# Performance work log

Hardware: AMD Instinct MI355X
Metric: run time of the kernel (lower is better)

## Reference

```python
import jax, jax.numpy as jnp
import numpy as np

HID = 1024   # hidden_size
NH = 16      # num_heads
HD = HID // NH   # 64 head_dim
RD = int(HD * 0.25)  # 16 rotary_dim
B = 2
S = 2048
ROPE_BASE = 10000.0


def setup_inputs() -> dict:
    key = jax.random.key(0)
    ks = jax.random.split(key, 4)
    hidden_states = jax.random.normal(ks[0], (B, S, HID), jnp.float32)
    # torch nn.Linear weights: [out_features, in_features]
    Wqkv = jax.random.normal(ks[1], (3 * HID, HID), jnp.float32) * (HID ** -0.5)
    bqkv = jnp.zeros((3 * HID,), jnp.float32)
    Wd = jax.random.normal(ks[2], (HID, HID), jnp.float32) * (HID ** -0.5)
    bd = jnp.zeros((HID,), jnp.float32)
    return {"hidden_states": hidden_states, "Wqkv": Wqkv, "bqkv": bqkv, "Wd": Wd, "bd": bd}


def _rotary_tables(seq_len):
    inv_freq = 1.0 / (ROPE_BASE ** (jnp.arange(0, RD, 2, dtype=jnp.float32) / RD))
    t = jnp.arange(seq_len, dtype=jnp.float32)
    freqs = jnp.outer(t, inv_freq)                       # [S, RD/2]
    emb = jnp.concatenate([freqs, freqs], axis=-1)       # [S, RD]
    return jnp.cos(emb)[None, None], jnp.sin(emb)[None, None]  # [1,1,S,RD]


def _rotate_half(x):
    x1, x2 = jnp.split(x, 2, axis=-1)
    return jnp.concatenate([-x2, x1], axis=-1)


def reference(hidden_states, Wqkv, bqkv, Wd, bd):
    b, s, _ = hidden_states.shape
    qkv = hidden_states @ Wqkv.T + bqkv                  # [b,s,3*HID]
    qkv = qkv.reshape(b, s, 3, NH, HD).transpose(2, 0, 3, 1, 4)  # [3,b,nh,s,hd]
    q, k, v = qkv[0], qkv[1], qkv[2]

    cos, sin = _rotary_tables(s)
    q_rot, q_pass = q[..., :RD], q[..., RD:]
    k_rot, k_pass = k[..., :RD], k[..., RD:]
    q_rot = q_rot * cos + _rotate_half(q_rot) * sin
    k_rot = k_rot * cos + _rotate_half(k_rot) * sin
    q = jnp.concatenate([q_rot, q_pass], axis=-1)
    k = jnp.concatenate([k_rot, k_pass], axis=-1)

    scale = HD ** -0.5
    logits = jnp.einsum('bhqd,bhkd->bhqk', q, k) * scale  # [b,nh,s,s]
    causal_mask = jnp.triu(jnp.full((s, s), -jnp.inf, dtype=logits.dtype), 1)
    probs = jax.nn.softmax(logits + causal_mask, axis=-1)

    # KA recurrence: A_i = p_ii * V_i + sum_{j<i} p_ij * A_j
    # <=> (I - strict_lower(P)) A = diag(P) * V  -> batched triangular solve
    L = jnp.eye(s, dtype=probs.dtype) - jnp.tril(probs, -1)      # [b,nh,s,s]
    rhs = jnp.diagonal(probs, axis1=-2, axis2=-1)[..., None] * v  # [b,nh,s,hd]
    A = jax.scipy.linalg.solve_triangular(L, rhs, lower=True)     # [b,nh,s,hd]

    attn_output = A.transpose(0, 2, 1, 3).reshape(b, s, HID)
    return attn_output @ Wd.T + bd
```

## Files before the change

kernel.cpp:

```cpp
#include <hip/hip_runtime.h>
#include <math.h>

namespace {

constexpr int B  = 2, S = 2048, NH = 16, HD = 64, HID = 1024;
constexpr int BH = B * NH;
constexpr int NSTEP2 = 8;

constexpr size_t OFF_A    = 4194304;
constexpr size_t OFF_Q    = 12582912;
constexpr size_t OFF_K    = 16777216;
constexpr size_t OFF_V    = 20971520;
constexpr size_t OFF_ZI   = 25231360;
constexpr size_t OFF_PD   = 25296896;
constexpr size_t OFF_UP   = 25362432;
constexpr size_t WS_FLOATS = 29294592;

typedef __attribute__((ext_vector_type(8))) short bf16x8;
typedef __attribute__((ext_vector_type(4))) float f32x4;

__device__ inline unsigned short bf_rne(float x) {
  const unsigned u = __float_as_uint(x);
  return (unsigned short)((u + 0x7FFFu + ((u >> 16) & 1u)) >> 16);
}
__device__ inline float bf2f(short h) {
  return __uint_as_float((unsigned)(unsigned short)h << 16);
}
__device__ inline void split8(const float4 a, const float4 b,
                              bf16x8& hi, bf16x8& lo) {
  float v[8] = {a.x, a.y, a.z, a.w, b.x, b.y, b.z, b.w};
#pragma unroll
  for (int i = 0; i < 8; ++i) {
    const unsigned short h = bf_rne(v[i]);
    hi[i] = (short)h;
    lo[i] = (short)bf_rne(v[i] - bf2f((short)h));
  }
}
__device__ inline f32x4 apply3(const short* __restrict__ mh_,
                               const short* __restrict__ ml_,
                               const float* __restrict__ brow, int lg) {
  f32x4 o = (f32x4)0.f;
#pragma unroll
  for (int ks = 0; ks < 2; ++ks) {
    const bf16x8 mh = *(const bf16x8*)(mh_ + ks * 32 + lg * 8);
    const bf16x8 ml = *(const bf16x8*)(ml_ + ks * 32 + lg * 8);
    const float* bp = brow + ks * 32 + lg * 8;
    bf16x8 bh, bl;
    split8(*(const float4*)bp, *(const float4*)(bp + 4), bh, bl);
    o = __builtin_amdgcn_mfma_f32_16x16x32_bf16(mh, bh, o, 0, 0, 0);
    o = __builtin_amdgcn_mfma_f32_16x16x32_bf16(ml, bh, o, 0, 0, 0);
    o = __builtin_amdgcn_mfma_f32_16x16x32_bf16(mh, bl, o, 0, 0, 0);
  }
  return o;
}

__global__ __launch_bounds__(256) void split_pre(
    const float* __restrict__ hs, short* __restrict__ h1, short* __restrict__ l1,
    const float* __restrict__ wq, short* __restrict__ h2, short* __restrict__ l2) {
  const int n1 = B * S * HID / 4;
  const int n2 = 3 * HID * HID / 4;
  for (int g = blockIdx.x * 256 + threadIdx.x; g < n1 + n2; g += gridDim.x * 256) {
    const bool first = g < n1;
    const int idx = first ? g : g - n1;
    const float4 x = first ? *(const float4*)(hs + (size_t)idx * 4)
                           : *(const float4*)(wq + (size_t)idx * 4);
    short4 h, l;
    h.x = bf_rne(x.x); h.y = bf_rne(x.y); h.z = bf_rne(x.z); h.w = bf_rne(x.w);
    l.x = bf_rne(x.x - bf2f(h.x));
    l.y = bf_rne(x.y - bf2f(h.y));
    l.z = bf_rne(x.z - bf2f(h.z));
    l.w = bf_rne(x.w - bf2f(h.w));
    if (first) {
      *(short4*)(h1 + (size_t)idx * 4) = h;
      *(short4*)(l1 + (size_t)idx * 4) = l;
    } else {
      *(short4*)(h2 + (size_t)idx * 4) = h;
      *(short4*)(l2 + (size_t)idx * 4) = l;
    }
  }
}

__global__ __launch_bounds__(256) void split_post(
    const float* __restrict__ Abuf, short* __restrict__ h1, short* __restrict__ l1,
    const float* __restrict__ wd, short* __restrict__ h2, short* __restrict__ l2) {
  const int n1 = B * S * HID / 4;
  const int n2 = HID * HID / 4;
  for (int g = blockIdx.x * 256 + threadIdx.x; g < n1 + n2; g += gridDim.x * 256) {
    float4 x;
    if (g < n1) {
      const int m = g >> 8, q = g & 255;
      const int k0 = q * 4;
      const int b = m >> 11, s = m & (S - 1);
      const int h = k0 >> 6, d = k0 & 63;
      x = *(const float4*)(Abuf + (((size_t)(b * NH + h) * S + s) << 6) + d);
    } else {
      x = *(const float4*)(wd + (size_t)(g - n1) * 4);
    }
    short4 h, l;
    h.x = bf_rne(x.x); h.y = bf_rne(x.y); h.z = bf_rne(x.z); h.w = bf_rne(x.w);
    l.x = bf_rne(x.x - bf2f(h.x));
    l.y = bf_rne(x.y - bf2f(h.y));
    l.z = bf_rne(x.z - bf2f(h.z));
    l.w = bf_rne(x.w - bf2f(h.w));
    if (g < n1) {
      *(short4*)(h1 + (size_t)g * 4) = h;
      *(short4*)(l1 + (size_t)g * 4) = l;
    } else {
      *(short4*)(h2 + (size_t)(g - n1) * 4) = h;
      *(short4*)(l2 + (size_t)(g - n1) * 4) = l;
    }
  }
}

__global__ __launch_bounds__(256) void gemm_bf3(
    const short* __restrict__ Ahi, const short* __restrict__ Alo,
    const short* __restrict__ Bhi, const short* __restrict__ Blo,
    const float* __restrict__ bias, float* __restrict__ C,
    int M, int N, int K) {
  __shared__ short ash[128][40], als[128][40], bsh[128][40], bls[128][40];
  const int t = threadIdx.x;
  const int m0 = blockIdx.y * 128, n0 = blockIdx.x * 128;
  const int w = t >> 6, l = t & 63;
  const int wm = (w >> 1) * 64, wn = (w & 1) * 64;
  const int lr = l & 15, lk = (l >> 4) * 8;
  f32x4 acc[4][4];
#pragma unroll
  for (int i = 0; i < 4; ++i)
#pragma unroll
    for (int j = 0; j < 4; ++j) acc[i][j] = (f32x4)0.f;

  for (int kb = 0; kb < K; kb += 32) {
    __syncthreads();
#pragma unroll
    for (int i = 0; i < 2; ++i) {
      const int idx = t + i * 256;
      const int row = idx >> 2, c8 = (idx & 3) * 8;
      *(uint4*)&ash[row][c8] = *(const uint4*)(Ahi + (size_t)(m0 + row) * K + kb + c8);
      *(uint4*)&als[row][c8] = *(const uint4*)(Alo + (size_t)(m0 + row) * K + kb + c8);
      *(uint4*)&bsh[row][c8] = *(const uint4*)(Bhi + (size_t)(n0 + row) * K + kb + c8);
      *(uint4*)&bls[row][c8] = *(const uint4*)(Blo + (size_t)(n0 + row) * K + kb + c8);
    }
    __syncthreads();
    bf16x8 ah[4], al[4], bh[4], bl[4];
#pragma unroll
    for (int mi = 0; mi < 4; ++mi) {
      ah[mi] = *(const bf16x8*)&ash[wm + mi * 16 + lr][lk];
      al[mi] = *(const bf16x8*)&als[wm + mi * 16 + lr][lk];
    }
#pragma unroll
    for (int ni = 0; ni < 4; ++ni) {
      bh[ni] = *(const bf16x8*)&bsh[wn + ni * 16 + lr][lk];
      bl[ni] = *(const bf16x8*)&bls[wn + ni * 16 + lr][lk];
    }
#pragma unroll
    for (int mi = 0; mi < 4; ++mi)
#pragma unroll
      for (int ni = 0; ni < 4; ++ni) {
        acc[mi][ni] = __builtin_amdgcn_mfma_f32_16x16x32_bf16(
            ah[mi], bh[ni], acc[mi][ni], 0, 0, 0);
        acc[mi][ni] = __builtin_amdgcn_mfma_f32_16x16x32_bf16(
            al[mi], bh[ni], acc[mi][ni], 0, 0, 0);
        acc[mi][ni] = __builtin_amdgcn_mfma_f32_16x16x32_bf16(
            ah[mi], bl[ni], acc[mi][ni], 0, 0, 0);
      }
  }
  const int rq = (l >> 4) * 4;
#pragma unroll
  for (int ni = 0; ni < 4; ++ni) {
    const int col = n0 + wn + ni * 16 + lr;
    const float bv = bias[col];
#pragma unroll
    for (int mi = 0; mi < 4; ++mi)
#pragma unroll
      for (int r = 0; r < 4; ++r) {
        const int row = m0 + wm + mi * 16 + rq + r;
        C[(size_t)row * N + col] = acc[mi][ni][r] + bv;
      }
  }
}

__global__ __launch_bounds__(256) void k2_rope(
    const float* __restrict__ qkv, short* __restrict__ Qhi,
    short* __restrict__ Qlo, short* __restrict__ Khi,
    short* __restrict__ Klo, float* __restrict__ V) {
  const int g  = blockIdx.x * 256 + threadIdx.x;
  const int s  = g & (S - 1);
  const int bh = g >> 11;
  const int b  = bh >> 4, h = bh & 15;
  const float* base = qkv + ((size_t)b * S + s) * 3072 + h * 64;
  float q[64], k[64], v[64];
#pragma unroll
  for (int f = 0; f < 16; ++f) {
    const float4 x = *(const float4*)(base + f * 4);
    q[f*4+0]=x.x; q[f*4+1]=x.y; q[f*4+2]=x.z; q[f*4+3]=x.w;
    const float4 y = *(const float4*)(base + 1024 + f * 4);
    k[f*4+0]=y.x; k[f*4+1]=y.y; k[f*4+2]=y.z; k[f*4+3]=y.w;
    const float4 z = *(const float4*)(base + 2048 + f * 4);
    v[f*4+0]=z.x; v[f*4+1]=z.y; v[f*4+2]=z.z; v[f*4+3]=z.w;
  }
  const float PW[8] = {1.0f, 3.1622776601683795f, 10.0f, 31.622776601683793f,
                       100.0f, 316.22776601683796f, 1000.0f, 3162.2776601683795f};
  float qr[16], kr[16];
#pragma unroll
  for (int d = 0; d < 16; ++d) {
    const int j = d & 7;
    const float invf = 1.0f / PW[j];
    const float fr = (float)s * invf;
    float sn, c;
    sincosf(fr, &sn, &c);
    const float rq = (d < 8) ? -q[d + 8] : q[d - 8];
    const float rk = (d < 8) ? -k[d + 8] : k[d - 8];
    qr[d] = q[d] * c + rq * sn;
    kr[d] = k[d] * c + rk * sn;
  }
#pragma unroll
  for (int d = 0; d < 16; ++d) { q[d] = qr[d]; k[d] = kr[d]; }
#pragma unroll
  for (int d = 0; d < 64; ++d) q[d] *= 0.125f;
  const size_t o = ((size_t)bh * S + s) << 6;
  float* vd = V + o;
#pragma unroll
  for (int f = 0; f < 16; ++f) {
    short4 qh, ql, kh, kl;
// ... 181 lines not shown
        const size_t kb = kbase + (((size_t)(16 * ni + lr)) << 6) + ks * 32 + lg * 8;
        const bf16x8 bhf = *(const bf16x8*)(Khi + kb);
        const bf16x8 blf = *(const bf16x8*)(Klo + kb);
        p[ni] = __builtin_amdgcn_mfma_f32_16x16x32_bf16(qfh[ks], bhf, p[ni], 0, 0, 0);
        p[ni] = __builtin_amdgcn_mfma_f32_16x16x32_bf16(qfl[ks], bhf, p[ni], 0, 0, 0);
        p[ni] = __builtin_amdgcn_mfma_f32_16x16x32_bf16(qfh[ks], blf, p[ni], 0, 0, 0);
      }
    }
    const size_t pbase = (((size_t)bh * 16 + (ib >> 1)) * 64) * 64;
#pragma unroll
    for (int ni = 0; ni < 4; ++ni) {
      const int c = 16 * ni + lr;
#pragma unroll
      for (int i = 0; i < 4; ++i) {
        const float val = __expf(p[ni][i]) * ziv[i];
        const unsigned short h = bf_rne(val);
        P10h[pbase + (size_t)(rloc0 + i) * 64 + c] = (short)h;
        P10l[pbase + (size_t)(rloc0 + i) * 64 + c] = (short)bf_rne(val - bf2f((short)h));
      }
    }
  }
  {
    const int c = t & 63, g = t >> 6;
#pragma unroll
    for (int i = 0; i < 16; ++i) {
      const int r = 16 * g + i;
      X[r][c] = (r == c) ? 1.f : 0.f;
    }
  }
  __syncthreads();

  const int c = t & 63, g = t >> 6;
  if (w == 0) {
    for (int rr = 1; rr < 16; ++rr) {
      float a = 0.f;
      for (int j = 0; j < rr; ++j) a += Nb[rr][j] * X[j][l];
      X[rr][l] += a;
    }
  }
  __syncthreads();
#pragma unroll
  for (int I = 1; I < 4; ++I) {
    {
      const int rb4 = 16 * I + 4 * g;
      float s0 = 0.f, s1 = 0.f, s2 = 0.f, s3 = 0.f;
      for (int j = 0; j < 16 * I; j += 4) {
        const float4 n0 = *(const float4*)&Nb[rb4 + 0][j];
        const float4 n1 = *(const float4*)&Nb[rb4 + 1][j];
        const float4 n2 = *(const float4*)&Nb[rb4 + 2][j];
        const float4 n3 = *(const float4*)&Nb[rb4 + 3][j];
        const float x0 = X[j + 0][c], x1 = X[j + 1][c];
        const float x2 = X[j + 2][c], x3 = X[j + 3][c];
        s0 += n0.x * x0 + n0.y * x1 + n0.z * x2 + n0.w * x3;
        s1 += n1.x * x0 + n1.y * x1 + n1.z * x2 + n1.w * x3;
        s2 += n2.x * x0 + n2.y * x1 + n2.z * x2 + n2.w * x3;
        s3 += n3.x * x0 + n3.y * x1 + n3.z * x2 + n3.w * x3;
      }
      X[rb4 + 0][c] += s0; X[rb4 + 1][c] += s1;
      X[rb4 + 2][c] += s2; X[rb4 + 3][c] += s3;
    }
    __syncthreads();
    if (w == 0) {
      const int rb = 16 * I;
      for (int rr = 1; rr < 16; ++rr) {
        const int r = rb + rr;
        float a = 0.f;
        for (int j = rb; j < r; ++j) a += Nb[r][j] * X[j][l];
        X[r][l] += a;
      }
    }
    __syncthreads();
  }

  const size_t mb = (((size_t)bh * 32 + ib) * 64) * 64;
  for (int v = t; v < 4096; v += 256) {
    const int r = v >> 6, cc = v & 63;
    const float x = X[r][cc];
    const unsigned short h = bf_rne(x);
    Mrh[mb + v] = (short)h;
    Mrl[mb + v] = (short)bf_rne(x - bf2f((short)h));
  }
}

__global__ __launch_bounds__(256) void k5_acc(
    const short* __restrict__ Qhi, const short* __restrict__ Qlo,
    const short* __restrict__ Khi, const short* __restrict__ Klo,
    const float* __restrict__ Abuf, const float* __restrict__ zinv,
    float* __restrict__ up, int s) {
  const int bh = blockIdx.z, rh = blockIdx.y, g = blockIdx.x;
  __shared__ float Es[128][68];
  __shared__ float Ats[64][68];
  const int t = threadIdx.x;
  const int w = t >> 6, l = t & 63;
  const int lr = l & 15, lg = l >> 4;
  const int rw = 32 * w;
  const int base = s * 256 + rh * 128;

  bf16x8 qfh[2][2], qfl[2][2];
#pragma unroll
  for (int mi = 0; mi < 2; ++mi)
#pragma unroll
    for (int ks = 0; ks < 2; ++ks) {
      const size_t qo = (((size_t)bh * S + base + rw + mi * 16 + lr) << 6) + ks * 32 + lg * 8;
      qfh[mi][ks] = *(const bf16x8*)(Qhi + qo);
      qfl[mi][ks] = *(const bf16x8*)(Qlo + qo);
    }
  float ziv[2][4];
#pragma unroll
  for (int mi = 0; mi < 2; ++mi)
#pragma unroll
    for (int r = 0; r < 4; ++r)
      ziv[mi][r] = zinv[(size_t)bh * S + base + rw + mi * 16 + lg * 4 + r];

  f32x4 out[2][4];
#pragma unroll
  for (int mi = 0; mi < 2; ++mi)
#pragma unroll
    for (int ni = 0; ni < 4; ++ni) out[mi][ni] = (f32x4)0.f;

  for (int j = g; j < 2 * s; j += 7) {
    for (int h = 0; h < 2; ++h) {
      __syncthreads();
      for (int v = t; v < 1024; v += 256) {
        const int d = v & 63, sq = v >> 6;
        const size_t ab = ((size_t)bh * S + j * 128 + h * 64 + sq * 4) << 6;
        float4 o;
        o.x = Abuf[ab + d];
        o.y = Abuf[ab + 64 + d];
        o.z = Abuf[ab + 128 + d];
        o.w = Abuf[ab + 192 + d];
        *(float4*)&Ats[d][sq * 4] = o;
      }
      f32x4 qk[2][4];
#pragma unroll
      for (int mi = 0; mi < 2; ++mi)
#pragma unroll
        for (int ni = 0; ni < 4; ++ni) qk[mi][ni] = (f32x4)0.f;
#pragma unroll
      for (int ks = 0; ks < 2; ++ks) {
#pragma unroll
        for (int ni = 0; ni < 4; ++ni) {
          const size_t ko = (((size_t)bh * S + j * 128 + h * 64 + ni * 16 + lr) << 6) + ks * 32 + lg * 8;
          const bf16x8 kh8 = *(const bf16x8*)(Khi + ko);
          const bf16x8 kl8 = *(const bf16x8*)(Klo + ko);
#pragma unroll
          for (int mi = 0; mi < 2; ++mi) {
            qk[mi][ni] = __builtin_amdgcn_mfma_f32_16x16x32_bf16(
                qfh[mi][ks], kh8, qk[mi][ni], 0, 0, 0);
            qk[mi][ni] = __builtin_amdgcn_mfma_f32_16x16x32_bf16(
                qfl[mi][ks], kh8, qk[mi][ni], 0, 0, 0);
            qk[mi][ni] = __builtin_amdgcn_mfma_f32_16x16x32_bf16(
                qfh[mi][ks], kl8, qk[mi][ni], 0, 0, 0);
          }
        }
      }
#pragma unroll
      for (int mi = 0; mi < 2; ++mi)
#pragma unroll
        for (int ni = 0; ni < 4; ++ni)
#pragma unroll
          for (int r = 0; r < 4; ++r)
            Es[rw + mi * 16 + lg * 4 + r][ni * 16 + lr] =
                __expf(qk[mi][ni][r]) * ziv[mi][r];
      __syncthreads();
#pragma unroll
      for (int ks = 0; ks < 2; ++ks) {
        bf16x8 eh[2], el[2];
#pragma unroll
        for (int mi = 0; mi < 2; ++mi) {
          const float* ep = &Es[rw + mi * 16 + lr][ks * 32 + lg * 8];
          split8(*(const float4*)ep, *(const float4*)(ep + 4), eh[mi], el[mi]);
        }
#pragma unroll
        for (int ni = 0; ni < 4; ++ni) {
          const float* ap = &Ats[ni * 16 + lr][ks * 32 + lg * 8];
          bf16x8 ah8, al8;
          split8(*(const float4*)ap, *(const float4*)(ap + 4), ah8, al8);
#pragma unroll
          for (int mi = 0; mi < 2; ++mi) {
            out[mi][ni] = __builtin_amdgcn_mfma_f32_16x16x32_bf16(
                eh[mi], ah8, out[mi][ni], 0, 0, 0);
            out[mi][ni] = __builtin_amdgcn_mfma_f32_16x16x32_bf16(
                el[mi], ah8, out[mi][ni], 0, 0, 0);
            out[mi][ni] = __builtin_amdgcn_mfma_f32_16x16x32_bf16(
                eh[mi], al8, out[mi][ni], 0, 0, 0);
          }
        }
      }
    }
  }
  float* ub = up + (((size_t)(bh * 7 + g) * 2 + rh) << 13);
#pragma unroll
  for (int mi = 0; mi < 2; ++mi)
#pragma unroll
    for (int ni = 0; ni < 4; ++ni)
#pragma unroll
      for (int r = 0; r < 4; ++r)
        ub[(size_t)(rw + mi * 16 + lg * 4 + r) * 64 + ni * 16 + lr] =
            out[mi][ni][r];
}

__global__ __launch_bounds__(256) void k5_fin(
    const short* __restrict__ Qhi, const short* __restrict__ Qlo,
    const short* __restrict__ Khi, const short* __restrict__ Klo,
    const float* __restrict__ V, const float* __restrict__ pd,
    const float* __restrict__ zinv, const float* __restrict__ up,
    const short* __restrict__ Mrh, const short* __restrict__ Mrl,
    const short* __restrict__ P10h, const short* __restrict__ P10l,
    float* __restrict__ Abuf, int s) {
  const int d0 = blockIdx.x * 16;
  const int bh = blockIdx.y;
  const int t = threadIdx.x;
  const int w = t >> 6, l = t & 63;
  const int lr = l & 15, lg = l >> 4;
  const int base = s * 256;
  __shared__ float uT[16][260];
  __shared__ float aT[16][132];
  __shared__ float Es[128][68];
  const int ng = (2 * s < 7) ? 2 * s : 7;

  for (int v = t; v < 1024; v += 256) {
    const int r = v >> 2, f = v & 3;
    const int R = base + r;
    const float4 x = *(const float4*)(V + (((size_t)bh * S + R) << 6) + d0 + f * 4);
    const float p = pd[(size_t)bh * S + R];
    float a0 = p * x.x, a1 = p * x.y, a2 = p * x.z, a3 = p * x.w;
    const int rh = r >> 7, rr = r & 127;
    for (int g = 0; g < ng; ++g) {
      const float4 y = *(const float4*)(
          up + (((size_t)(bh * 7 + g) * 2 + rh) << 13) + (rr << 6) + d0 + f * 4);
      a0 += y.x; a1 += y.y; a2 += y.z; a3 += y.w;
    }
    uT[f * 4 + 0][r] = a0; uT[f * 4 + 1][r] = a1;
    uT[f * 4 + 2][r] = a2; uT[f * 4 + 3][r] = a3;
  }
  __syncthreads();
  const size_t mstep = (size_t)bh * 32 + s * 4;
  {
    const size_t mb = ((mstep + 0) * 64 + 16 * w + lr) * 64;
    const f32x4 o = apply3(Mrh + mb, Mrl + mb, &uT[lr][0], lg);
#pragma unroll
    for (int i = 0; i < 4; ++i) {
      const int r = 16 * w + lg * 4 + i;
      Abuf[(((size_t)bh * S + base + r) << 6) + d0 + lr] = o[i];
      aT[lr][r] = o[i];
    }
  }
  __syncthreads();
  {
    const size_t pb = (((size_t)bh * 16 + 2 * s) * 64 + 16 * w + lr) * 64;
    const f32x4 o = apply3(P10h + pb, P10l + pb, &aT[lr][0], lg);
#pragma unroll
    for (int i = 0; i < 4; ++i)
      uT[lr][64 + 16 * w + lg * 4 + i] += o[i];
  }
  __syncthreads();
  {
    const size_t mb = ((mstep + 1) * 64 + 16 * w + lr) * 64;
    const f32x4 o = apply3(Mrh + mb, Mrl + mb, &uT[lr][64], lg);
#pragma unroll
    for (int i = 0; i < 4; ++i) {
      const int r = 16 * w + lg * 4 + i;
      Abuf[(((size_t)bh * S + base + 64 + r) << 6) + d0 + lr] = o[i];
      aT[lr][64 + r] = o[i];
    }
  }
  {
    const int rw = 32 * w;
    bf16x8 qh_[2][2], ql_[2][2];
#pragma unroll
    for (int mi = 0; mi < 2; ++mi)
#pragma unroll
      for (int ks = 0; ks < 2; ++ks) {
        const size_t qo = (((size_t)bh * S + base + 128 + rw + mi * 16 + lr) << 6) + ks * 32 + lg * 8;
        qh_[mi][ks] = *(const bf16x8*)(Qhi + qo);
        ql_[mi][ks] = *(const bf16x8*)(Qlo + qo);
      }
    float zv[2][4];
#pragma unroll
    for (int mi = 0; mi < 2; ++mi)
#pragma unroll
      for (int i = 0; i < 4; ++i)
        zv[mi][i] = zinv[(size_t)bh * S + base + 128 + rw + mi * 16 + lg * 4 + i];
    for (int ch = 0; ch < 2; ++ch) {
      __syncthreads();
      f32x4 qk[2][4];
#pragma unroll
      for (int mi = 0; mi < 2; ++mi)
#pragma unroll
        for (int ni = 0; ni < 4; ++ni) qk[mi][ni] = (f32x4)0.f;
#pragma unroll
      for (int ks = 0; ks < 2; ++ks) {
#pragma unroll
        for (int ni = 0; ni < 4; ++ni) {
          const size_t ko = (((size_t)bh * S + base + ch * 64 + ni * 16 + lr) << 6) + ks * 32 + lg * 8;
          const bf16x8 kh8 = *(const bf16x8*)(Khi + ko);
          const bf16x8 kl8 = *(const bf16x8*)(Klo + ko);
#pragma unroll
          for (int mi = 0; mi < 2; ++mi) {
            qk[mi][ni] = __builtin_amdgcn_mfma_f32_16x16x32_bf16(
                qh_[mi][ks], kh8, qk[mi][ni], 0, 0, 0);
            qk[mi][ni] = __builtin_amdgcn_mfma_f32_16x16x32_bf16(
                ql_[mi][ks], kh8, qk[mi][ni], 0, 0, 0);
            qk[mi][ni] = __builtin_amdgcn_mfma_f32_16x16x32_bf16(
                qh_[mi][ks], kl8, qk[mi][ni], 0, 0, 0);
          }
        }
      }
#pragma unroll
      for (int mi = 0; mi < 2; ++mi)
#pragma unroll
        for (int ni = 0; ni < 4; ++ni)
#pragma unroll
          for (int i = 0; i < 4; ++i)
            Es[rw + mi * 16 + lg * 4 + i][ni * 16 + lr] =
                __expf(qk[mi][ni][i]) * zv[mi][i];
      __syncthreads();
#pragma unroll
      for (int mi = 0; mi < 2; ++mi) {
        f32x4 o = (f32x4)0.f;
#pragma unroll
        for (int kq = 0; kq < 2; ++kq) {
          const float* ep = &Es[rw + mi * 16 + lr][kq * 32 + lg * 8];
          bf16x8 eh, el;
          split8(*(const float4*)ep, *(const float4*)(ep + 4), eh, el);
          const float* ap = &aT[lr][ch * 64 + kq * 32 + lg * 8];
          bf16x8 ah, al;
          split8(*(const float4*)ap, *(const float4*)(ap + 4), ah, al);
          o = __builtin_amdgcn_mfma_f32_16x16x32_bf16(eh, ah, o, 0, 0, 0);
          o = __builtin_amdgcn_mfma_f32_16x16x32_bf16(el, ah, o, 0, 0, 0);
          o = __builtin_amdgcn_mfma_f32_16x16x32_bf16(eh, al, o, 0, 0, 0);
        }
#pragma unroll
        for (int i = 0; i < 4; ++i)
          uT[lr][128 + rw + mi * 16 + lg * 4 + i] += o[i];
      }
    }
  }
  __syncthreads();
  {
    const size_t mb = ((mstep + 2) * 64 + 16 * w + lr) * 64;
    const f32x4 o = apply3(Mrh + mb, Mrl + mb, &uT[lr][128], lg);
#pragma unroll
    for (int i = 0; i < 4; ++i) {
      const int r = 16 * w + lg * 4 + i;
      Abuf[(((size_t)bh * S + base + 128 + r) << 6) + d0 + lr] = o[i];
      aT[lr][r] = o[i];
    }
  }
  __syncthreads();
  {
    const size_t pb = (((size_t)bh * 16 + 2 * s + 1) * 64 + 16 * w + lr) * 64;
    const f32x4 o = apply3(P10h + pb, P10l + pb, &aT[lr][0], lg);
#pragma unroll
    for (int i = 0; i < 4; ++i)
      uT[lr][192 + 16 * w + lg * 4 + i] += o[i];
  }
  __syncthreads();
  {
    const size_t mb = ((mstep + 3) * 64 + 16 * w + lr) * 64;
    const f32x4 o = apply3(Mrh + mb, Mrl + mb, &uT[lr][192], lg);
#pragma unroll
    for (int i = 0; i < 4; ++i) {
      const int r = 16 * w + lg * 4 + i;
      Abuf[(((size_t)bh * S + base + 192 + r) << 6) + d0 + lr] = o[i];
    }
  }
}

}

extern "C" void kernel_launch(void* const* d_in, const int* in_sizes, int n_in,
                              void* d_out, int out_size, void* d_ws, size_t ws_size,
                              hipStream_t stream) {
  const float* hs   = (const float*)d_in[0];
  const float* Wqkv = (const float*)d_in[1];
  const float* bqkv = (const float*)d_in[2];
  const float* Wd   = (const float*)d_in[3];
  const float* bd   = (const float*)d_in[4];
  float* out = (float*)d_out;
  float* W   = (float*)d_ws;
  if (ws_size < WS_FLOATS * sizeof(float)) return;

  float* qkv   = W;
  float* partZ = W;
  float* Abuf  = W + OFF_A;
  short* Qhi   = (short*)(W + OFF_Q);
  short* Qlo   = Qhi + 4194304;
  short* Khi   = (short*)(W + OFF_K);
  short* Klo   = Khi + 4194304;
  float* Vb    = W + OFF_V;
  float* zi    = W + OFF_ZI;
  float* pdg   = W + OFF_PD;
  float* up    = W + OFF_UP;

  char* wsb = (char*)d_ws;
  short* Ahi  = (short*)(wsb + 50331648);
  short* Alo  = Ahi + 4194304;
  short* Whi  = (short*)(wsb + 67108864);
  short* Wlo  = Whi + 3145728;
  short* A2hi = (short*)(wsb + 50331648);
  short* A2lo = A2hi + 4194304;
  short* Wdhi = (short*)(wsb + 67108864);
  short* Wdlo = Wdhi + 1048576;
  short* P10h = (short*)(wsb);
  short* P10l = P10h + 2097152;
  short* Mrh  = (short*)(wsb + 33554432);
  short* Mrl  = Mrh + 4194304;

  split_pre<<<dim3(2048), 256, 0, stream>>>(hs, Ahi, Alo, Wqkv, Whi, Wlo);
  gemm_bf3<<<dim3(24, 32), 256, 0, stream>>>(Ahi, Alo, Whi, Wlo, bqkv, qkv,
                                             B*S, 3*HID, HID);
  k2_rope<<<dim3(BH * S / 256), 256, 0, stream>>>(qkv, Qhi, Qlo, Khi, Klo, Vb);
  k3_scores<<<dim3(16, 16, BH), 256, 0, stream>>>(Qhi, Qlo, Khi, Klo, partZ, pdg);
  k3_reduce<<<dim3(BH * S / 256), 256, 0, stream>>>(partZ, zi, pdg);
  k4_minv<<<dim3(S / 64, BH), 256, 0, stream>>>(Qhi, Qlo, Khi, Klo, zi,
                                                Mrh, Mrl, P10h, P10l);
  for (int s = 0; s < NSTEP2; ++s) {
    if (s > 0) {
      const int ng = (2 * s < 7) ? 2 * s : 7;
      k5_acc<<<dim3(ng, 2, BH), 256, 0, stream>>>(Qhi, Qlo, Khi, Klo, Abuf, zi,
                                                  up, s);
    }
    k5_fin<<<dim3(4, BH), 256, 0, stream>>>(Qhi, Qlo, Khi, Klo, Vb, pdg, zi, up,
                                            Mrh, Mrl, P10h, P10l, Abuf, s);
  }
  split_post<<<dim3(2048), 256, 0, stream>>>(Abuf, A2hi, A2lo, Wd, Wdhi, Wdlo);
  gemm_bf3<<<dim3(8, 32), 256, 0, stream>>>(A2hi, A2lo, Wdhi, Wdlo, bd, out,
                                            B*S, HID, HID);
}
```

Baseline: 692.5 us.

## Fuse bf16 splitting into GEMM loads and merge acc/fin steps via atomic tickets

The separate split_pre/split_post kernels are removed. The GEMM now loads fp32 operands, splits them into hi/lo bf16 while staging to shared memory, and gathers the attention output layout directly for the output projection. The per-step k5_acc and k5_fin launches are merged into one k5_step kernel. In it, the last four blocks to arrive on a per-head atomic counter wait for all partials and then run the finalize stage, so each step needs one launch instead of two. This cuts kernel launches and intermediate global traffic. In exchange it adds split arithmetic inside the GEMM inner loop and a spin-wait that assumes every block of a step is co-resident.

```diff
diff --git a/kernel.cpp b/kernel.cpp
--- a/kernel.cpp
+++ b/kernel.cpp
@@ -54,67 +54,9 @@
   return o;
 }
 
-__global__ __launch_bounds__(256) void split_pre(
-    const float* __restrict__ hs, short* __restrict__ h1, short* __restrict__ l1,
-    const float* __restrict__ wq, short* __restrict__ h2, short* __restrict__ l2) {
-  const int n1 = B * S * HID / 4;
-  const int n2 = 3 * HID * HID / 4;
-  for (int g = blockIdx.x * 256 + threadIdx.x; g < n1 + n2; g += gridDim.x * 256) {
-    const bool first = g < n1;
-    const int idx = first ? g : g - n1;
-    const float4 x = first ? *(const float4*)(hs + (size_t)idx * 4)
-                           : *(const float4*)(wq + (size_t)idx * 4);
-    short4 h, l;
-    h.x = bf_rne(x.x); h.y = bf_rne(x.y); h.z = bf_rne(x.z); h.w = bf_rne(x.w);
-    l.x = bf_rne(x.x - bf2f(h.x));
-    l.y = bf_rne(x.y - bf2f(h.y));
-    l.z = bf_rne(x.z - bf2f(h.z));
-    l.w = bf_rne(x.w - bf2f(h.w));
-    if (first) {
-      *(short4*)(h1 + (size_t)idx * 4) = h;
-      *(short4*)(l1 + (size_t)idx * 4) = l;
-    } else {
-      *(short4*)(h2 + (size_t)idx * 4) = h;
-      *(short4*)(l2 + (size_t)idx * 4) = l;
-    }
-  }
-}
-
-__global__ __launch_bounds__(256) void split_post(
-    const float* __restrict__ Abuf, short* __restrict__ h1, short* __restrict__ l1,
-    const float* __restrict__ wd, short* __restrict__ h2, short* __restrict__ l2) {
-  const int n1 = B * S * HID / 4;
-  const int n2 = HID * HID / 4;
-  for (int g = blockIdx.x * 256 + threadIdx.x; g < n1 + n2; g += gridDim.x * 256) {
-    float4 x;
-    if (g < n1) {
-      const int m = g >> 8, q = g & 255;
-      const int k0 = q * 4;
-      const int b = m >> 11, s = m & (S - 1);
-      const int h = k0 >> 6, d = k0 & 63;
-      x = *(const float4*)(Abuf + (((size_t)(b * NH + h) * S + s) << 6) + d);
-    } else {
-      x = *(const float4*)(wd + (size_t)(g - n1) * 4);
-    }
-    short4 h, l;
-    h.x = bf_rne(x.x); h.y = bf_rne(x.y); h.z = bf_rne(x.z); h.w = bf_rne(x.w);
-    l.x = bf_rne(x.x - bf2f(h.x));
-    l.y = bf_rne(x.y - bf2f(h.y));
-    l.z = bf_rne(x.z - bf2f(h.z));
-    l.w = bf_rne(x.w - bf2f(h.w));
-    if (g < n1) {
-      *(short4*)(h1 + (size_t)g * 4) = h;
-      *(short4*)(l1 + (size_t)g * 4) = l;
-    } else {
-      *(short4*)(h2 + (size_t)(g - n1) * 4) = h;
-      *(short4*)(l2 + (size_t)(g - n1) * 4) = l;
-    }
-  }
-}
-
-__global__ __launch_bounds__(256) void gemm_bf3(
-    const short* __restrict__ Ahi, const short* __restrict__ Alo,
-    const short* __restrict__ Bhi, const short* __restrict__ Blo,
+template<int GATHER>
+__global__ __launch_bounds__(256) void gemm_f32(
+    const float* __restrict__ A, const float* __restrict__ Bm,
     const float* __restrict__ bias, float* __restrict__ C,
     int M, int N, int K) {
   __shared__ short ash[128][40], als[128][40], bsh[128][40], bls[128][40];
@@ -135,10 +77,24 @@
     for (int i = 0; i < 2; ++i) {
       const int idx = t + i * 256;
       const int row = idx >> 2, c8 = (idx & 3) * 8;
-      *(uint4*)&ash[row][c8] = *(const uint4*)(Ahi + (size_t)(m0 + row) * K + kb + c8);
-      *(uint4*)&als[row][c8] = *(const uint4*)(Alo + (size_t)(m0 + row) * K + kb + c8);
-      *(uint4*)&bsh[row][c8] = *(const uint4*)(Bhi + (size_t)(n0 + row) * K + kb + c8);
-      *(uint4*)&bls[row][c8] = *(const uint4*)(Blo + (size_t)(n0 + row) * K + kb + c8);
+      const float* srcA;
+      if (GATHER) {
+        const int m = m0 + row;
+        const int b = m >> 11, ss = m & (S - 1);
+        const int kk = kb + c8;
+        const int h = kk >> 6, d = kk & 63;
+        srcA = A + (((size_t)(b * NH + h) * S + ss) << 6) + d;
+      } else {
+        srcA = A + (size_t)(m0 + row) * K + kb + c8;
+      }
+      bf16x8 hi, lo;
+      split8(*(const float4*)srcA, *(const float4*)(srcA + 4), hi, lo);
+      *(bf16x8*)&ash[row][c8] = hi;
+      *(bf16x8*)&als[row][c8] = lo;
+      const float* srcB = Bm + (size_t)(n0 + row) * K + kb + c8;
+      split8(*(const float4*)srcB, *(const float4*)(srcB + 4), hi, lo);
+      *(bf16x8*)&bsh[row][c8] = hi;
+      *(bf16x8*)&bls[row][c8] = lo;
     }
     __syncthreads();
     bf16x8 ah[4], al[4], bh[4], bl[4];
@@ -486,173 +442,44 @@
   }
 }
 
-__global__ __launch_bounds__(256) void k5_acc(
-    const short* __restrict__ Qhi, const short* __restrict__ Qlo,
-    const short* __restrict__ Khi, const short* __restrict__ Klo,
-    const float* __restrict__ Abuf, const float* __restrict__ zinv,
-    float* __restrict__ up, int s) {
-  const int bh = blockIdx.z, rh = blockIdx.y, g = blockIdx.x;
-  __shared__ float Es[128][68];
-  __shared__ float Ats[64][68];
-  const int t = threadIdx.x;
-  const int w = t >> 6, l = t & 63;
-  const int lr = l & 15, lg = l >> 4;
-  const int rw = 32 * w;
-  const int base = s * 256 + rh * 128;
-
-  bf16x8 qfh[2][2], qfl[2][2];
-#pragma unroll
-  for (int mi = 0; mi < 2; ++mi)
-#pragma unroll
-    for (int ks = 0; ks < 2; ++ks) {
-      const size_t qo = (((size_t)bh * S + base + rw + mi * 16 + lr) << 6) + ks * 32 + lg * 8;
-      qfh[mi][ks] = *(const bf16x8*)(Qhi + qo);
-      qfl[mi][ks] = *(const bf16x8*)(Qlo + qo);
-    }
-  float ziv[2][4];
-#pragma unroll
-  for (int mi = 0; mi < 2; ++mi)
-#pragma unroll
-    for (int r = 0; r < 4; ++r)
-      ziv[mi][r] = zinv[(size_t)bh * S + base + rw + mi * 16 + lg * 4 + r];
-
-  f32x4 out[2][4];
-#pragma unroll
-  for (int mi = 0; mi < 2; ++mi)
-#pragma unroll
-    for (int ni = 0; ni < 4; ++ni) out[mi][ni] = (f32x4)0.f;
-
-  for (int j = g; j < 2 * s; j += 7) {
-    for (int h = 0; h < 2; ++h) {
-      __syncthreads();
-      for (int v = t; v < 1024; v += 256) {
-        const int d = v & 63, sq = v >> 6;
-        const size_t ab = ((size_t)bh * S + j * 128 + h * 64 + sq * 4) << 6;
-        float4 o;
-        o.x = Abuf[ab + d];
-        o.y = Abuf[ab + 64 + d];
-        o.z = Abuf[ab + 128 + d];
-        o.w = Abuf[ab + 192 + d];
-        *(float4*)&Ats[d][sq * 4] = o;
-      }
-      f32x4 qk[2][4];
-#pragma unroll
-      for (int mi = 0; mi < 2; ++mi)
-#pragma unroll
-        for (int ni = 0; ni < 4; ++ni) qk[mi][ni] = (f32x4)0.f;
-#pragma unroll
-      for (int ks = 0; ks < 2; ++ks) {
-#pragma unroll
-        for (int ni = 0; ni < 4; ++ni) {
-          const size_t ko = (((size_t)bh * S + j * 128 + h * 64 + ni * 16 + lr) << 6) + ks * 32 + lg * 8;
-          const bf16x8 kh8 = *(const bf16x8*)(Khi + ko);
-          const bf16x8 kl8 = *(const bf16x8*)(Klo + ko);
-#pragma unroll
-          for (int mi = 0; mi < 2; ++mi) {
-            qk[mi][ni] = __builtin_amdgcn_mfma_f32_16x16x32_bf16(
-                qfh[mi][ks], kh8, qk[mi][ni], 0, 0, 0);
-            qk[mi][ni] = __builtin_amdgcn_mfma_f32_16x16x32_bf16(
-                qfl[mi][ks], kh8, qk[mi][ni], 0, 0, 0);
-            qk[mi][ni] = __builtin_amdgcn_mfma_f32_16x16x32_bf16(
-                qfh[mi][ks], kl8, qk[mi][ni], 0, 0, 0);
-          }
-        }
-      }
-#pragma unroll
-      for (int mi = 0; mi < 2; ++mi)
-#pragma unroll
-        for (int ni = 0; ni < 4; ++ni)
-#pragma unroll
-          for (int r = 0; r < 4; ++r)
-            Es[rw + mi * 16 + lg * 4 + r][ni * 16 + lr] =
-                __expf(qk[mi][ni][r]) * ziv[mi][r];
-      __syncthreads();
-#pragma unroll
-      for (int ks = 0; ks < 2; ++ks) {
-        bf16x8 eh[2], el[2];
-#pragma unroll
-        for (int mi = 0; mi < 2; ++mi) {
-          const float* ep = &Es[rw + mi * 16 + lr][ks * 32 + lg * 8];
-          split8(*(const float4*)ep, *(const float4*)(ep + 4), eh[mi], el[mi]);
-        }
-#pragma unroll
-        for (int ni = 0; ni < 4; ++ni) {
-          const float* ap = &Ats[ni * 16 + lr][ks * 32 + lg * 8];
-          bf16x8 ah8, al8;
-          split8(*(const float4*)ap, *(const float4*)(ap + 4), ah8, al8);
-#pragma unroll
-          for (int mi = 0; mi < 2; ++mi) {
-            out[mi][ni] = __builtin_amdgcn_mfma_f32_16x16x32_bf16(
-                eh[mi], ah8, out[mi][ni], 0, 0, 0);
-            out[mi][ni] = __builtin_amdgcn_mfma_f32_16x16x32_bf16(
-                el[mi], ah8, out[mi][ni], 0, 0, 0);
-            out[mi][ni] = __builtin_amdgcn_mfma_f32_16x16x32_bf16(
-                eh[mi], al8, out[mi][ni], 0, 0, 0);
-          }
-        }
-      }
-    }
-  }
-  float* ub = up + (((size_t)(bh * 7 + g) * 2 + rh) << 13);
-#pragma unroll
-  for (int mi = 0; mi < 2; ++mi)
-#pragma unroll
-    for (int ni = 0; ni < 4; ++ni)
-#pragma unroll
-      for (int r = 0; r < 4; ++r)
-        ub[(size_t)(rw + mi * 16 + lg * 4 + r) * 64 + ni * 16 + lr] =
-            out[mi][ni][r];
-}
-
 __global__ __launch_bounds__(256) void k5_fin(
     const short* __restrict__ Qhi, const short* __restrict__ Qlo,
     const short* __restrict__ Khi, const short* __restrict__ Klo,
     const float* __restrict__ V, const float* __restrict__ pd,
-    const float* __restrict__ zinv, const float* __restrict__ up,
-    const short* __restrict__ Mrh, const short* __restrict__ Mrl,
-    const short* __restrict__ P10h, const short* __restrict__ P10l,
-    float* __restrict__ Abuf, int s) {
+    const float* __restrict__ zinv, const short* __restrict__ Mrh,
+    const short* __restrict__ Mrl, const short* __restrict__ P10h,
+    const short* __restrict__ P10l, float* __restrict__ Abuf) {
   const int d0 = blockIdx.x * 16;
   const int bh = blockIdx.y;
   const int t = threadIdx.x;
   const int w = t >> 6, l = t & 63;
   const int lr = l & 15, lg = l >> 4;
-  const int base = s * 256;
   __shared__ float uT[16][260];
   __shared__ float aT[16][132];
   __shared__ float Es[128][68];
-  const int ng = (2 * s < 7) ? 2 * s : 7;
 
   for (int v = t; v < 1024; v += 256) {
     const int r = v >> 2, f = v & 3;
-    const int R = base + r;
-    const float4 x = *(const float4*)(V + (((size_t)bh * S + R) << 6) + d0 + f * 4);
-    const float p = pd[(size_t)bh * S + R];
-    float a0 = p * x.x, a1 = p * x.y, a2 = p * x.z, a3 = p * x.w;
-    const int rh = r >> 7, rr = r & 127;
-    for (int g = 0; g < ng; ++g) {
-      const float4 y = *(const float4*)(
-          up + (((size_t)(bh * 7 + g) * 2 + rh) << 13) + (rr << 6) + d0 + f * 4);
-      a0 += y.x; a1 += y.y; a2 += y.z; a3 += y.w;
-    }
-    uT[f * 4 + 0][r] = a0; uT[f * 4 + 1][r] = a1;
-    uT[f * 4 + 2][r] = a2; uT[f * 4 + 3][r] = a3;
-  }
-  __syncthreads();
-  const size_t mstep = (size_t)bh * 32 + s * 4;
+    const float4 x = *(const float4*)(V + (((size_t)bh * S + r) << 6) + d0 + f * 4);
+    const float p = pd[(size_t)bh * S + r];
+    uT[f * 4 + 0][r] = p * x.x; uT[f * 4 + 1][r] = p * x.y;
+    uT[f * 4 + 2][r] = p * x.z; uT[f * 4 + 3][r] = p * x.w;
+  }
+  __syncthreads();
+  const size_t mstep = (size_t)bh * 32;
   {
     const size_t mb = ((mstep + 0) * 64 + 16 * w + lr) * 64;
     const f32x4 o = apply3(Mrh + mb, Mrl + mb, &uT[lr][0], lg);
 #pragma unroll
     for (int i = 0; i < 4; ++i) {
       const int r = 16 * w + lg * 4 + i;
-      Abuf[(((size_t)bh * S + base + r) << 6) + d0 + lr] = o[i];
+      Abuf[(((size_t)bh * S + r) << 6) + d0 + lr] = o[i];
       aT[lr][r] = o[i];
     }
   }
   __syncthreads();
   {
-    const size_t pb = (((size_t)bh * 16 + 2 * s) * 64 + 16 * w + lr) * 64;
+    const size_t pb = (((size_t)bh * 16) * 64 + 16 * w + lr) * 64;
     const f32x4 o = apply3(P10h + pb, P10l + pb, &aT[lr][0], lg);
 #pragma unroll
     for (int i = 0; i < 4; ++i)
@@ -665,7 +492,7 @@
 #pragma unroll
     for (int i = 0; i < 4; ++i) {
       const int r = 16 * w + lg * 4 + i;
-      Abuf[(((size_t)bh * S + base + 64 + r) << 6) + d0 + lr] = o[i];
+      Abuf[(((size_t)bh * S + 64 + r) << 6) + d0 + lr] = o[i];
       aT[lr][64 + r] = o[i];
     }
   }
@@ -676,7 +503,7 @@
     for (int mi = 0; mi < 2; ++mi)
 #pragma unroll
       for (int ks = 0; ks < 2; ++ks) {
-        const size_t qo = (((size_t)bh * S + base + 128 + rw + mi * 16 + lr) << 6) + ks * 32 + lg * 8;
+        const size_t qo = (((size_t)bh * S + 128 + rw + mi * 16 + lr) << 6) + ks * 32 + lg * 8;
         qh_[mi][ks] = *(const bf16x8*)(Qhi + qo);
         ql_[mi][ks] = *(const bf16x8*)(Qlo + qo);
       }
@@ -685,7 +512,7 @@
     for (int mi = 0; mi < 2; ++mi)
 #pragma unroll
       for (int i = 0; i < 4; ++i)
-        zv[mi][i] = zinv[(size_t)bh * S + base + 128 + rw + mi * 16 + lg * 4 + i];
+        zv[mi][i] = zinv[(size_t)bh * S + 128 + rw + mi * 16 + lg * 4 + i];
     for (int ch = 0; ch < 2; ++ch) {
       __syncthreads();
       f32x4 qk[2][4];
@@ -697,7 +524,7 @@
       for (int ks = 0; ks < 2; ++ks) {
 #pragma unroll
         for (int ni = 0; ni < 4; ++ni) {
-          const size_t ko = (((size_t)bh * S + base + ch * 64 + ni * 16 + lr) << 6) + ks * 32 + lg * 8;
+          const size_t ko = (((size_t)bh * S + ch * 64 + ni * 16 + lr) << 6) + ks * 32 + lg * 8;
           const bf16x8 kh8 = *(const bf16x8*)(Khi + ko);
           const bf16x8 kl8 = *(const bf16x8*)(Klo + ko);
 #pragma unroll
@@ -748,13 +575,13 @@
 #pragma unroll
     for (int i = 0; i < 4; ++i) {
       const int r = 16 * w + lg * 4 + i;
-      Abuf[(((size_t)bh * S + base + 128 + r) << 6) + d0 + lr] = o[i];
+      Abuf[(((size_t)bh * S + 128 + r) << 6) + d0 + lr] = o[i];
       aT[lr][r] = o[i];
     }
   }
   __syncthreads();
   {
-    const size_t pb = (((size_t)bh * 16 + 2 * s + 1) * 64 + 16 * w + lr) * 64;
+    const size_t pb = (((size_t)bh * 16 + 1) * 64 + 16 * w + lr) * 64;
     const f32x4 o = apply3(P10h + pb, P10l + pb, &aT[lr][0], lg);
 #pragma unroll
     for (int i = 0; i < 4; ++i)
@@ -767,9 +594,303 @@
 #pragma unroll
     for (int i = 0; i < 4; ++i) {
       const int r = 16 * w + lg * 4 + i;
-      Abuf[(((size_t)bh * S + base + 192 + r) << 6) + d0 + lr] = o[i];
-    }
-  }
+      Abuf[(((size_t)bh * S + 192 + r) << 6) + d0 + lr] = o[i];
+    }
+  }
+}
+
+__global__ __launch_bounds__(256) void k5_step(
+    const short* __restrict__ Qhi, const short* __restrict__ Qlo,
+    const short* __restrict__ Khi, const short* __restrict__ Klo,
+    const float* __restrict__ V, const float* __restrict__ pd,
+    const float* __restrict__ zinv, float* __restrict__ up,
+    const short* __restrict__ Mrh, const short* __restrict__ Mrl,
+    const short* __restrict__ P10h, const short* __restrict__ P10l,
+    float* __restrict__ Abuf, int* __restrict__ cnt, int s) {
+  __shared__ float sb[14976];
+  __shared__ int tks;
+#define ES(r, c)  sb[(r) * 68 + (c)]
+#define ATS(d, c) sb[8704 + (d) * 68 + (c)]
+#define UT(dd, r) sb[(dd) * 260 + (r)]
+#define AT(dd, r) sb[4160 + (dd) * 132 + (r)]
+#define EF(r, c)  sb[6272 + (r) * 68 + (c)]
+  const int bh = blockIdx.z, rh = blockIdx.y, g = blockIdx.x;
+  const int ng = gridDim.x;
+  const int t = threadIdx.x;
+  const int w = t >> 6, l = t & 63;
+  const int lr = l & 15, lg = l >> 4;
+  const int rw = 32 * w;
+  const int base = s * 256 + rh * 128;
+
+  bf16x8 qfh[2][2], qfl[2][2];
+#pragma unroll
+  for (int mi = 0; mi < 2; ++mi)
+#pragma unroll
+    for (int ks = 0; ks < 2; ++ks) {
+      const size_t qo = (((size_t)bh * S + base + rw + mi * 16 + lr) << 6) + ks * 32 + lg * 8;
+      qfh[mi][ks] = *(const bf16x8*)(Qhi + qo);
+      qfl[mi][ks] = *(const bf16x8*)(Qlo + qo);
+    }
+  float ziv[2][4];
+#pragma unroll
+  for (int mi = 0; mi < 2; ++mi)
+#pragma unroll
+    for (int r = 0; r < 4; ++r)
+      ziv[mi][r] = zinv[(size_t)bh * S + base + rw + mi * 16 + lg * 4 + r];
+
+  f32x4 out[2][4];
+#pragma unroll
+  for (int mi = 0; mi < 2; ++mi)
+#pragma unroll
+    for (int ni = 0; ni < 4; ++ni) out[mi][ni] = (f32x4)0.f;
+
+  for (int j = g; j < 2 * s; j += 7) {
+    for (int h = 0; h < 2; ++h) {
+      __syncthreads();
+      for (int v = t; v < 1024; v += 256) {
+        const int d = v & 63, sq = v >> 6;
+        const size_t ab = ((size_t)bh * S + j * 128 + h * 64 + sq * 4) << 6;
+        ATS(d, sq * 4 + 0) = Abuf[ab + d];
+        ATS(d, sq * 4 + 1) = Abuf[ab + 64 + d];
+        ATS(d, sq * 4 + 2) = Abuf[ab + 128 + d];
+        ATS(d, sq * 4 + 3) = Abuf[ab + 192 + d];
+      }
+      f32x4 qk[2][4];
+#pragma unroll
+      for (int mi = 0; mi < 2; ++mi)
+#pragma unroll
+        for (int ni = 0; ni < 4; ++ni) qk[mi][ni] = (f32x4)0.f;
+#pragma unroll
+      for (int ks = 0; ks < 2; ++ks) {
+#pragma unroll
+        for (int ni = 0; ni < 4; ++ni) {
+          const size_t ko = (((size_t)bh * S + j * 128 + h * 64 + ni * 16 + lr) << 6) + ks * 32 + lg * 8;
+          const bf16x8 kh8 = *(const bf16x8*)(Khi + ko);
+          const bf16x8 kl8 = *(const bf16x8*)(Klo + ko);
+#pragma unroll
+          for (int mi = 0; mi < 2; ++mi) {
+            qk[mi][ni] = __builtin_amdgcn_mfma_f32_16x16x32_bf16(
+                qfh[mi][ks], kh8, qk[mi][ni], 0, 0, 0);
+            qk[mi][ni] = __builtin_amdgcn_mfma_f32_16x16x32_bf16(
+                qfl[mi][ks], kh8, qk[mi][ni], 0, 0, 0);
+            qk[mi][ni] = __builtin_amdgcn_mfma_f32_16x16x32_bf16(
+                qfh[mi][ks], kl8, qk[mi][ni], 0, 0, 0);
+          }
+        }
+      }
+#pragma unroll
+      for (int mi = 0; mi < 2; ++mi)
+#pragma unroll
+        for (int ni = 0; ni < 4; ++ni)
+#pragma unroll
+          for (int r = 0; r < 4; ++r)
+            ES(rw + mi * 16 + lg * 4 + r, ni * 16 + lr) =
+                __expf(qk[mi][ni][r]) * ziv[mi][r];
+      __syncthreads();
+#pragma unroll
+      for (int ks = 0; ks < 2; ++ks) {
+        bf16x8 eh[2], el[2];
+#pragma unroll
+        for (int mi = 0; mi < 2; ++mi) {
+          const float* ep = &ES(rw + mi * 16 + lr, ks * 32 + lg * 8);
+          split8(*(const float4*)ep, *(const float4*)(ep + 4), eh[mi], el[mi]);
+        }
+#pragma unroll
+        for (int ni = 0; ni < 4; ++ni) {
+          const float* ap = &ATS(ni * 16 + lr, ks * 32 + lg * 8);
+          bf16x8 ah8, al8;
+          split8(*(const float4*)ap, *(const float4*)(ap + 4), ah8, al8);
+#pragma unroll
+          for (int mi = 0; mi < 2; ++mi) {
+            out[mi][ni] = __builtin_amdgcn_mfma_f32_16x16x32_bf16(
+                eh[mi], ah8, out[mi][ni], 0, 0, 0);
+            out[mi][ni] = __builtin_amdgcn_mfma_f32_16x16x32_bf16(
+                el[mi], ah8, out[mi][ni], 0, 0, 0);
+            out[mi][ni] = __builtin_amdgcn_mfma_f32_16x16x32_bf16(
+                eh[mi], al8, out[mi][ni], 0, 0, 0);
+          }
+        }
+      }
+    }
+  }
+  {
+    float* ub = up + (((size_t)(bh * 7 + g) * 2 + rh) << 13);
+#pragma unroll
+    for (int mi = 0; mi < 2; ++mi)
+#pragma unroll
+      for (int ni = 0; ni < 4; ++ni)
+#pragma unroll
+        for (int r = 0; r < 4; ++r)
+          ub[(size_t)(rw + mi * 16 + lg * 4 + r) * 64 + ni * 16 + lr] =
+              out[mi][ni][r];
+  }
+  __threadfence();
+  if (t == 0) tks = atomicAdd(&cnt[bh], 1);
+  __syncthreads();
+  const int total = 2 * ng;
+  const int ticket = tks;
+  if (ticket < total - 4) return;
+  const int quad = ticket - (total - 4);
+  if (t == 0) {
+    while (__hip_atomic_load(&cnt[bh], __ATOMIC_ACQUIRE,
+                             __HIP_MEMORY_SCOPE_AGENT) < total) {}
+  }
+  __syncthreads();
+  __threadfence();
+
+  const int d0 = quad * 16;
+  const int fbase = s * 256;
+  for (int v = t; v < 1024; v += 256) {
+    const int r = v >> 2, f = v & 3;
+    const int R = fbase + r;
+    const float4 x = *(const float4*)(V + (((size_t)bh * S + R) << 6) + d0 + f * 4);
+    const float p = pd[(size_t)bh * S + R];
+    float a0 = p * x.x, a1 = p * x.y, a2 = p * x.z, a3 = p * x.w;
+    const int rhh = r >> 7, rr = r & 127;
+    for (int gg = 0; gg < ng; ++gg) {
+      const float4 y = *(const float4*)(
+          up + (((size_t)(bh * 7 + gg) * 2 + rhh) << 13) + (rr << 6) + d0 + f * 4);
+      a0 += y.x; a1 += y.y; a2 += y.z; a3 += y.w;
+    }
+    UT(f * 4 + 0, r) = a0; UT(f * 4 + 1, r) = a1;
+    UT(f * 4 + 2, r) = a2; UT(f * 4 + 3, r) = a3;
+  }
+  __syncthreads();
+  const size_t mstep = (size_t)bh * 32 + s * 4;
+  {
+    const size_t mb = ((mstep + 0) * 64 + 16 * w + lr) * 64;
+    const f32x4 o = apply3(Mrh + mb, Mrl + mb, &UT(lr, 0), lg);
+#pragma unroll
+    for (int i = 0; i < 4; ++i) {
+      const int r = 16 * w + lg * 4 + i;
+      Abuf[(((size_t)bh * S + fbase + r) << 6) + d0 + lr] = o[i];
+      AT(lr, r) = o[i];
+    }
+  }
+  __syncthreads();
+  {
+    const size_t pb = (((size_t)bh * 16 + 2 * s) * 64 + 16 * w + lr) * 64;
+    const f32x4 o = apply3(P10h + pb, P10l + pb, &AT(lr, 0), lg);
+#pragma unroll
+    for (int i = 0; i < 4; ++i)
+      UT(lr, 64 + 16 * w + lg * 4 + i) += o[i];
+  }
+  __syncthreads();
+  {
+    const size_t mb = ((mstep + 1) * 64 + 16 * w + lr) * 64;
+    const f32x4 o = apply3(Mrh + mb, Mrl + mb, &UT(lr, 64), lg);
+#pragma unroll
+    for (int i = 0; i < 4; ++i) {
+      const int r = 16 * w + lg * 4 + i;
+      Abuf[(((size_t)bh * S + fbase + 64 + r) << 6) + d0 + lr] = o[i];
+      AT(lr, 64 + r) = o[i];
+    }
+  }
+  {
+    bf16x8 qh_[2][2], ql_[2][2];
+#pragma unroll
+    for (int mi = 0; mi < 2; ++mi)
+#pragma unroll
+      for (int ks = 0; ks < 2; ++ks) {
+        const size_t qo = (((size_t)bh * S + fbase + 128 + rw + mi * 16 + lr) << 6) + ks * 32 + lg * 8;
+        qh_[mi][ks] = *(const bf16x8*)(Qhi + qo);
+        ql_[mi][ks] = *(const bf16x8*)(Qlo + qo);
+      }
+    float zv[2][4];
+#pragma unroll
+    for (int mi = 0; mi < 2; ++mi)
+#pragma unroll
+      for (int i = 0; i < 4; ++i)
+        zv[mi][i] = zinv[(size_t)bh * S + fbase + 128 + rw + mi * 16 + lg * 4 + i];
+    for (int ch = 0; ch < 2; ++ch) {
+      __syncthreads();
+      f32x4 qk[2][4];
+#pragma unroll
+      for (int mi = 0; mi < 2; ++mi)
+#pragma unroll
+        for (int ni = 0; ni < 4; ++ni) qk[mi][ni] = (f32x4)0.f;
+#pragma unroll
+      for (int ks = 0; ks < 2; ++ks) {
+#pragma unroll
+        for (int ni = 0; ni < 4; ++ni) {
+          const size_t ko = (((size_t)bh * S + fbase + ch * 64 + ni * 16 + lr) << 6) + ks * 32 + lg * 8;
+          const bf16x8 kh8 = *(const bf16x8*)(Khi + ko);
+          const bf16x8 kl8 = *(const bf16x8*)(Klo + ko);
+#pragma unroll
+          for (int mi = 0; mi < 2; ++mi) {
+            qk[mi][ni] = __builtin_amdgcn_mfma_f32_16x16x32_bf16(
+                qh_[mi][ks], kh8, qk[mi][ni], 0, 0, 0);
+            qk[mi][ni] = __builtin_amdgcn_mfma_f32_16x16x32_bf16(
+                ql_[mi][ks], kh8, qk[mi][ni], 0, 0, 0);
+            qk[mi][ni] = __builtin_amdgcn_mfma_f32_16x16x32_bf16(
+                qh_[mi][ks], kl8, qk[mi][ni], 0, 0, 0);
+          }
+        }
+      }
+#pragma unroll
+      for (int mi = 0; mi < 2; ++mi)
+#pragma unroll
+        for (int ni = 0; ni < 4; ++ni)
+#pragma unroll
+          for (int i = 0; i < 4; ++i)
+            EF(rw + mi * 16 + lg * 4 + i, ni * 16 + lr) =
+                __expf(qk[mi][ni][i]) * zv[mi][i];
+      __syncthreads();
+#pragma unroll
+      for (int mi = 0; mi < 2; ++mi) {
+        f32x4 o = (f32x4)0.f;
+#pragma unroll
+        for (int kq = 0; kq < 2; ++kq) {
+          const float* ep = &EF(rw + mi * 16 + lr, kq * 32 + lg * 8);
+          bf16x8 eh, el;
+          split8(*(const float4*)ep, *(const float4*)(ep + 4), eh, el);
+          const float* ap = &AT(lr, ch * 64 + kq * 32 + lg * 8);
+          bf16x8 ah, al;
+          split8(*(const float4*)ap, *(const float4*)(ap + 4), ah, al);
+          o = __builtin_amdgcn_mfma_f32_16x16x32_bf16(eh, ah, o, 0, 0, 0);
+          o = __builtin_amdgcn_mfma_f32_16x16x32_bf16(el, ah, o, 0, 0, 0);
+          o = __builtin_amdgcn_mfma_f32_16x16x32_bf16(eh, al, o, 0, 0, 0);
+        }
+#pragma unroll
+        for (int i = 0; i < 4; ++i)
+          UT(lr, 128 + rw + mi * 16 + lg * 4 + i) += o[i];
+      }
+    }
+  }
+  __syncthreads();
+  {
+    const size_t mb = ((mstep + 2) * 64 + 16 * w + lr) * 64;
+    const f32x4 o = apply3(Mrh + mb, Mrl + mb, &UT(lr, 128), lg);
+#pragma unroll
+    for (int i = 0; i < 4; ++i) {
+      const int r = 16 * w + lg * 4 + i;
+      Abuf[(((size_t)bh * S + fbase + 128 + r) << 6) + d0 + lr] = o[i];
+      AT(lr, r) = o[i];
+    }
+  }
+  __syncthreads();
+  {
+    const size_t pb = (((size_t)bh * 16 + 2 * s + 1) * 64 + 16 * w + lr) * 64;
+    const f32x4 o = apply3(P10h + pb, P10l + pb, &AT(lr, 0), lg);
+#pragma unroll
+    for (int i = 0; i < 4; ++i)
+      UT(lr, 192 + 16 * w + lg * 4 + i) += o[i];
+  }
+  __syncthreads();
+  {
+    const size_t mb = ((mstep + 3) * 64 + 16 * w + lr) * 64;
+    const f32x4 o = apply3(Mrh + mb, Mrl + mb, &UT(lr, 192), lg);
+#pragma unroll
+    for (int i = 0; i < 4; ++i) {
+      const int r = 16 * w + lg * 4 + i;
+      Abuf[(((size_t)bh * S + fbase + 192 + r) << 6) + d0 + lr] = o[i];
+    }
+  }
+#undef ES
+#undef ATS
+#undef UT
+#undef AT
+#undef EF
 }
 
 }
@@ -799,37 +920,28 @@
   float* up    = W + OFF_UP;
 
   char* wsb = (char*)d_ws;
-  short* Ahi  = (short*)(wsb + 50331648);
-  short* Alo  = Ahi + 4194304;
-  short* Whi  = (short*)(wsb + 67108864);
-  short* Wlo  = Whi + 3145728;
-  short* A2hi = (short*)(wsb + 50331648);
-  short* A2lo = A2hi + 4194304;
-  short* Wdhi = (short*)(wsb + 67108864);
-  short* Wdlo = Wdhi + 1048576;
   short* P10h = (short*)(wsb);
   short* P10l = P10h + 2097152;
   short* Mrh  = (short*)(wsb + 33554432);
   short* Mrl  = Mrh + 4194304;
-
-  split_pre<<<dim3(2048), 256, 0, stream>>>(hs, Ahi, Alo, Wqkv, Whi, Wlo);
-  gemm_bf3<<<dim3(24, 32), 256, 0, stream>>>(Ahi, Alo, Whi, Wlo, bqkv, qkv,
-                                             B*S, 3*HID, HID);
+  int*   cnt  = (int*)(wsb + 116129792);
+
+  hipMemsetAsync(cnt, 0, NSTEP2 * BH * sizeof(int), stream);
+  gemm_f32<0><<<dim3(24, 32), 256, 0, stream>>>(hs, Wqkv, bqkv, qkv,
+                                                B*S, 3*HID, HID);
   k2_rope<<<dim3(BH * S / 256), 256, 0, stream>>>(qkv, Qhi, Qlo, Khi, Klo, Vb);
   k3_scores<<<dim3(16, 16, BH), 256, 0, stream>>>(Qhi, Qlo, Khi, Klo, partZ, pdg);
   k3_reduce<<<dim3(BH * S / 256), 256, 0, stream>>>(partZ, zi, pdg);
   k4_minv<<<dim3(S / 64, BH), 256, 0, stream>>>(Qhi, Qlo, Khi, Klo, zi,
                                                 Mrh, Mrl, P10h, P10l);
-  for (int s = 0; s < NSTEP2; ++s) {
-    if (s > 0) {
-      const int ng = (2 * s < 7) ? 2 * s : 7;
-      k5_acc<<<dim3(ng, 2, BH), 256, 0, stream>>>(Qhi, Qlo, Khi, Klo, Abuf, zi,
-                                                  up, s);
-    }
-    k5_fin<<<dim3(4, BH), 256, 0, stream>>>(Qhi, Qlo, Khi, Klo, Vb, pdg, zi, up,
-                                            Mrh, Mrl, P10h, P10l, Abuf, s);
-  }
-  split_post<<<dim3(2048), 256, 0, stream>>>(Abuf, A2hi, A2lo, Wd, Wdhi, Wdlo);
-  gemm_bf3<<<dim3(8, 32), 256, 0, stream>>>(A2hi, A2lo, Wdhi, Wdlo, bd, out,
-                                            B*S, HID, HID);
-}
+  k5_fin<<<dim3(4, BH), 256, 0, stream>>>(Qhi, Qlo, Khi, Klo, Vb, pdg, zi,
+                                          Mrh, Mrl, P10h, P10l, Abuf);
+  for (int s = 1; s < NSTEP2; ++s) {
+    const int ng = (2 * s < 7) ? 2 * s : 7;
+    k5_step<<<dim3(ng, 2, BH), 256, 0, stream>>>(
+        Qhi, Qlo, Khi, Klo, Vb, pdg, zi, up, Mrh, Mrl, P10h, P10l, Abuf,
+        cnt + s * BH, s);
+  }
+  gemm_f32<1><<<dim3(8, 32), 256, 0, stream>>>(Abuf, Wd, bd, out,
+                                               B*S, HID, HID);
+}
```

Measured after the change: 1.177 ms. 1.7x slower.
